# Performance work log

Hardware: AMD Instinct MI355X
Metric: run time of the kernel (lower is better)

Reference implementation:

```python
import jax, jax.numpy as jnp
import numpy as np
import math

N = 500_000
C_IN = 16
C_OUT = 64
H, W = 256, 256
PE_DIM = 32
BOUNDS = (-1.0, 1.0)
LN_EPS = 1e-5


def setup_inputs() -> dict:
    key = jax.random.key(0)
    ks = jax.random.split(key, 4)
    d_in = C_IN + 6 * PE_DIM  # 208
    pos = jax.random.uniform(ks[0], (N, 3), jnp.float32, minval=-1.0, maxval=1.0)
    features = jax.random.normal(ks[1], (N, C_IN), jnp.float32)
    W1 = jax.random.normal(ks[2], (d_in, C_OUT), jnp.float32) * (1.0 / math.sqrt(d_in))
    b1 = jnp.zeros((C_OUT,), jnp.float32)
    ln_g = jnp.ones((C_OUT,), jnp.float32)
    ln_b = jnp.zeros((C_OUT,), jnp.float32)
    W2 = jax.random.normal(ks[3], (C_OUT, C_OUT), jnp.float32) * (1.0 / math.sqrt(C_OUT))
    b2 = jnp.zeros((C_OUT,), jnp.float32)
    return {"pos": pos, "features": features, "W1": W1, "b1": b1,
            "ln_g": ln_g, "ln_b": ln_b, "W2": W2, "b2": b2,
            "axis1": 0, "axis2": 1}


def _pos_encode(pos):
    # sinusoidal encoding: per spatial dim, sin/cos at PE_DIM frequencies
    scale = BOUNDS[1] - BOUNDS[0]
    freq_bands = jnp.arange(PE_DIM, dtype=jnp.float32) / PE_DIM  # linspace(0,31,32)/32
    freqs = (pos / scale)[..., None] * (2.0 ** freq_bands) * math.pi  # [N,3,PE]
    # ordering per dim: sin_d, cos_d -> [N, 3*2*PE]
    enc = jnp.stack([jnp.sin(freqs), jnp.cos(freqs)], axis=2)  # [N,3,2,PE]
    return enc.reshape(pos.shape[0], 3 * 2 * PE_DIM)


def _layernorm(x, g, b):
    mu = jnp.mean(x, axis=-1, keepdims=True)
    var = jnp.var(x, axis=-1, keepdims=True)
    return (x - mu) * jax.lax.rsqrt(var + LN_EPS) * g + b


def reference(pos, features, W1, b1, ln_g, ln_b, W2, b2, axis1, axis2):
    # MLP on [features | pos_encoding]
    combined = jnp.concatenate([features, _pos_encode(pos)], axis=-1)  # [N,208]
    h = combined @ W1 + b1
    h = jax.nn.gelu(_layernorm(h, ln_g, ln_b), approximate=False)
    feat = h @ W2 + b2  # [N,C_OUT]

    # grid indices for the projected plane
    lo, hi = BOUNDS
    norm = jnp.clip((pos - lo) / (hi - lo), 0.0, 1.0)
    res = jnp.array([H, W], jnp.float32)
    i1 = jnp.clip(jnp.floor(norm[:, axis1] * res[0]), 0, H - 1).astype(jnp.int32)
    i2 = jnp.clip(jnp.floor(norm[:, axis2] * res[1]), 0, W - 1).astype(jnp.int32)
    flat = i1 * W + i2  # [N]

    # scatter-mean into grid
    sums = jax.ops.segment_sum(feat, flat, num_segments=H * W)  # [H*W, C]
    counts = jax.ops.segment_sum(jnp.ones((feat.shape[0],), jnp.float32), flat,
                                 num_segments=H * W)
    grid = sums / jnp.maximum(counts, 1.0)[:, None]  # [H*W, C]
    grid = grid.reshape(H, W, C_OUT).transpose(2, 0, 1)  # [C,H,W]
    return grid[None]  # [1,C,H,W]
```

## Files before the change

kernel.cpp:

```cpp
#include <hip/hip_runtime.h>
#include <math.h>

#define NPTS   500000
#define CIN    16
#define COUT   64
#define PE     32
#define GRID_H 256
#define GRID_W 256
#define NCELL  (GRID_H * GRID_W)

#define WS_HIST   0
#define WS_CUR    262144
#define WS_STARTS 524288
#define WS_RANK   786432
#define WS_WPK    2883456
#define WS_PART   2920320
#define WS_FEAT   2921344
#define WS_NEED   (WS_FEAT + (size_t)NPTS * COUT * 2)

#define PT_BLOCKS ((NPTS + 255) / 256)
#define MB_BLOCKS ((NPTS + 511) / 512)

#define W_HALFS   18432
#define W1_FRAGS  28
#define H_STRIDE  72
#define PS_WAVE   (16 * H_STRIDE)

typedef _Float16 f16x8 __attribute__((ext_vector_type(8)));
typedef _Float16 f16x2 __attribute__((ext_vector_type(2)));
typedef float    f32x4 __attribute__((ext_vector_type(4)));

__device__ __forceinline__ f16x2 pk2(float a, float b) {
    auto r = __builtin_amdgcn_cvt_pkrtz(a, b);
    union { decltype(r) x; f16x2 y; } u; u.x = r;
    return u.y;
}

__device__ __forceinline__ int cell_index(float v) {
    float nf = fminf(fmaxf((v + 1.0f) * 0.5f, 0.0f), 1.0f);
    int i = (int)floorf(nf * 256.0f);
    return i > 255 ? 255 : i;
}

__device__ __forceinline__ int flat_of(const float* pos, int p, int a1, int a2) {
    float pa1 = pos[p * 3 + a1];
    float pa2 = pos[p * 3 + a2];
    return cell_index(pa1) * GRID_W + cell_index(pa2);
}

__global__ void pack_hist_kernel(const float* __restrict__ W1,
                                 const float* __restrict__ W2,
                                 const float* __restrict__ pos,
                                 const int* __restrict__ ax1p,
                                 const int* __restrict__ ax2p,
                                 _Float16* __restrict__ wpk,
                                 unsigned int* __restrict__ hist,
                                 unsigned short* __restrict__ cellp)
{
    int i = blockIdx.x * 256 + threadIdx.x;
    if (i < W_HALFS) {
        int j = i & 7, lane = (i >> 3) & 63, f = i >> 9;
        int k  = ((f < W1_FRAGS) ? (f >> 2) : ((f - W1_FRAGS) >> 2)) * 32 + ((lane >> 4) << 3) + j;
        int ch = (f & 3) * 16 + (lane & 15);
        float v;
        if (f < W1_FRAGS) v = (k < 208) ? W1[k * 64 + ch] : 0.0f;
        else              v = W2[k * 64 + ch];
        wpk[i] = (_Float16)v;
    }
    if (i < NPTS) {
        int flat = flat_of(pos, i, ax1p[0], ax2p[0]);
        atomicAdd(&hist[flat], 1u);
        if (cellp) cellp[i] = (unsigned short)flat;
    }
}

__global__ void scan_sum_kernel(const unsigned int* __restrict__ hist,
                                unsigned int* __restrict__ part)
{
    __shared__ unsigned int sc[256];
    const int t = threadIdx.x;
    sc[t] = hist[blockIdx.x * 256 + t];
    __syncthreads();
    for (int off = 128; off > 0; off >>= 1) {
        if (t < off) sc[t] += sc[t + off];
        __syncthreads();
    }
    if (t == 0) part[blockIdx.x] = sc[0];
}

__global__ void scan_top_kernel(unsigned int* __restrict__ part)
{
    __shared__ unsigned int sc[256];
    const int t = threadIdx.x;
    unsigned int v = part[t];
    sc[t] = v;
    __syncthreads();
    for (int off = 1; off < 256; off <<= 1) {
        unsigned int add = (t >= off) ? sc[t - off] : 0u;
        __syncthreads();
        sc[t] += add;
        __syncthreads();
    }
    part[t] = sc[t] - v;
}

__global__ void scan_apply_kernel(const unsigned int* __restrict__ hist,
                                  const unsigned int* __restrict__ part,
                                  unsigned int* __restrict__ cur,
                                  unsigned int* __restrict__ starts)
{
    __shared__ unsigned int sc[256];
    const int t = threadIdx.x;
    unsigned int v = hist[blockIdx.x * 256 + t];
    sc[t] = v;
    __syncthreads();
    for (int off = 1; off < 256; off <<= 1) {
        unsigned int add = (t >= off) ? sc[t - off] : 0u;
        __syncthreads();
        sc[t] += add;
        __syncthreads();
    }
    unsigned int e = sc[t] - v + part[blockIdx.x];
    cur[blockIdx.x * 256 + t]    = e;
    starts[blockIdx.x * 256 + t] = e;
}

__global__ void scatter_kernel(const unsigned short* __restrict__ cellp,
                               unsigned int* __restrict__ cur,
                               int* __restrict__ rank)
{
    int p = blockIdx.x * 256 + threadIdx.x;
    if (p >= NPTS) return;
    int flat = cellp[p];
    rank[p] = (int)atomicAdd(&cur[flat], 1u);
}

__global__ __launch_bounds__(512, 4)
void mlp_mfma_kernel(const float* __restrict__ pos,
                     const float* __restrict__ feats,
                     const _Float16* __restrict__ wpk,
                     const float* __restrict__ b1,
                     const float* __restrict__ ln_g,
                     const float* __restrict__ ln_b,
                     const int*   __restrict__ ax1p,
                     const int*   __restrict__ ax2p,
                     const int*   __restrict__ rank,
                     _Float16* __restrict__ featbuf,
                     float* __restrict__ out,
                     int use_feat)
{
    __shared__ __align__(16) _Float16 WF[W_HALFS];
    __shared__ __align__(16) _Float16 PS[8 * PS_WAVE];

    {
        const uint4* src = (const uint4*)wpk;
        uint4* dst = (uint4*)WF;
        for (int i = threadIdx.x; i < W_HALFS / 8; i += 512) dst[i] = src[i];
    }

    const int lane = threadIdx.x & 63;
    const int wv   = threadIdx.x >> 6;
    const int g    = lane >> 4;
    const int n    = lane & 15;
    _Float16* Pw = PS + wv * PS_WAVE;

    int a1 = 0, a2 = 1;
    if (!use_feat) { a1 = ax1p[0]; a2 = ax2p[0]; }

    float b1v[4], lgv[4], lbv[4];
    #pragma unroll
    for (int c = 0; c < 4; ++c) {
        int ch = n + 16 * c;
        b1v[c] = b1[ch]; lgv[c] = ln_g[ch]; lbv[c] = ln_b[ch];
    }

    float ppx[4], ppy[4], ppz[4];
    const int wbase = blockIdx.x * 512 + wv * 64;
    int pt[4];
    #pragma unroll
    for (int t = 0; t < 4; ++t) {
        int st = wbase + t * 16 + n;
        int p  = (st < NPTS) ? st : 0;
        pt[t]  = p;
        ppx[t] = pos[3 * p + 0];
        ppy[t] = pos[3 * p + 1];
        ppz[t] = pos[3 * p + 2];
    }

    float4 fA[4], fB[4];
    if (g < 2) {
        #pragma unroll
        for (int t = 0; t < 4; ++t) {
            const float4* fr = (const float4*)(feats + (size_t)pt[t] * CIN + g * 8);
            fA[t] = fr[0]; fB[t] = fr[1];
        }
    }

    __syncthreads();

    f32x4 acc[4][4];
    #pragma unroll
    for (int t = 0; t < 4; ++t)
        #pragma unroll
        for (int c = 0; c < 4; ++c)
            acc[t][c] = (f32x4){0.0f, 0.0f, 0.0f, 0.0f};

    #pragma unroll
    for (int s = 0; s < 7; ++s) {
        const int k0 = s * 32 + g * 8;
        const bool isfeat = (s == 0) && (g < 2);
        const bool iszero = (k0 >= 208);
        float base = 0.0f, off = 0.0f; int d = 0;
        if (!isfeat && !iszero) {
            int e  = k0 - 16;
            d      = e >> 6;
            off    = ((e >> 5) & 1) ? 1.57079632679489662f : 0.0f;
            base   = 1.57079632679489662f * exp2f((float)(e & 31) * 0.03125f);
        }
        f16x8 af[4];
        #pragma unroll
        for (int t = 0; t < 4; ++t) {
            union { f16x8 v; f16x2 h[4]; } U;
            if (isfeat) {
                U.h[0] = pk2(fA[t].x, fA[t].y);
                U.h[1] = pk2(fA[t].z, fA[t].w);
                U.h[2] = pk2(fB[t].x, fB[t].y);
                U.h[3] = pk2(fB[t].z, fB[t].w);
            } else if (iszero) {
                #pragma unroll
                for (int q = 0; q < 4; ++q) U.h[q] = pk2(0.0f, 0.0f);
            } else {
                float pv  = (d == 0) ? ppx[t] : ((d == 1) ? ppy[t] : ppz[t]);
                float ang = pv * base;
                #pragma unroll
                for (int q = 0; q < 4; ++q) {
                    float v0 = __sinf(ang + off); ang *= 1.02189714865411668f;
                    float v1 = __sinf(ang + off); ang *= 1.02189714865411668f;
                    U.h[q] = pk2(v0, v1);
                }
            }
            af[t] = U.v;
        }
        #pragma unroll
        for (int c = 0; c < 4; ++c) {
            f16x8 bf = ((const f16x8*)WF)[(s * 4 + c) * 64 + lane];
            #pragma unroll
            for (int t = 0; t < 4; ++t)
                acc[t][c] = __builtin_amdgcn_mfma_f32_16x16x32_f16(af[t], bf, acc[t][c], 0, 0, 0);
        }
    }

    #pragma unroll
    for (int t = 0; t < 4; ++t) {
        f32x4 s1 = (f32x4){0.0f, 0.0f, 0.0f, 0.0f};
        f32x4 s2 = (f32x4){0.0f, 0.0f, 0.0f, 0.0f};
        #pragma unroll
        for (int c = 0; c < 4; ++c) {
            #pragma unroll
            for (int r = 0; r < 4; ++r) {
                float x = acc[t][c][r] + b1v[c];
                acc[t][c][r] = x;
                s1[r] += x;
                s2[r] += x * x;
            }
        }
        #pragma unroll
        for (int m = 1; m <= 8; m <<= 1) {
            #pragma unroll
            for (int r = 0; r < 4; ++r) {
                s1[r] += __shfl_xor(s1[r], m);
                s2[r] += __shfl_xor(s2[r], m);
            }
        }
        #pragma unroll
        for (int r = 0; r < 4; ++r) {
            float mu   = s1[r] * (1.0f / 64.0f);
            float var  = s2[r] * (1.0f / 64.0f) - mu * mu;
            float rstd = __builtin_amdgcn_rsqf(var + 1e-5f);
            int lrow = 4 * g + r;
            #pragma unroll
            for (int c = 0; c < 4; ++c) {
                float x  = (acc[t][c][r] - mu) * rstd * lgv[c] + lbv[c];
                float u  = x * (0.7978845608028654f + 0.0356774081363001f * x * x);
                float e  = __expf(2.0f * u);
                float th = 1.0f - 2.0f * __builtin_amdgcn_rcpf(e + 1.0f);
                float gv = 0.5f * x * (1.0f + th);
                Pw[lrow * H_STRIDE + n + 16 * c] = (_Float16)gv;
            }
        }

        f32x4 acc2[4];
        #pragma unroll
        for (int c = 0; c < 4; ++c) acc2[c] = (f32x4){0.0f, 0.0f, 0.0f, 0.0f};
        #pragma unroll
        for (int s = 0; s < 2; ++s) {
            f16x8 a2f = *(const f16x8*)(Pw + n * H_STRIDE + s * 32 + g * 8);
            #pragma unroll
            for (int c = 0; c < 4; ++c) {
                f16x8 bf = ((const f16x8*)WF)[(W1_FRAGS + s * 4 + c) * 64 + lane];
                acc2[c] = __builtin_amdgcn_mfma_f32_16x16x32_f16(a2f, bf, acc2[c], 0, 0, 0);
            }
        }

        #pragma unroll
        for (int r = 0; r < 4; ++r) {
            int lrow = 4 * g + r;
            #pragma unroll
            for (int c = 0; c < 4; ++c)
                Pw[lrow * H_STRIDE + n + 16 * c] = (_Float16)acc2[c][r];
        }

        if (use_feat) {
            int lrow  = lane >> 2;
            int gslot = wbase + t * 16 + lrow;
            if (gslot < NPTS) {
                int dst = rank[gslot];
                const uint4* src = (const uint4*)(Pw + lrow * H_STRIDE + (lane & 3) * 16);
                uint4* dstp = (uint4*)(featbuf + (size_t)dst * COUT + (lane & 3) * 16);
                dstp[0] = src[0];
                dstp[1] = src[1];
            }
        } else {
            int lrow = lane >> 2;
            int gp   = wbase + t * 16 + lrow;
            if (gp < NPTS) {
                int cellr = flat_of(pos, gp, a1, a2);
                const _Float16* srch = Pw + lrow * H_STRIDE;
                #pragma unroll
                for (int q = 0; q < 16; ++q) {
                    int ch = (lane & 3) * 16 + q;
                    unsafeAtomicAdd(&out[(size_t)ch * NCELL + cellr], (float)srch[ch]);
                }
            }
        }
    }
}

__global__ __launch_bounds__(256)
void reduce_kernel(const _Float16* __restrict__ featbuf,
                   const unsigned int* __restrict__ starts,
                   const unsigned int* __restrict__ hist,
                   const float* __restrict__ b2,
                   float* __restrict__ out)
{
    __shared__ float R[32][65];
    const int lane  = threadIdx.x & 63;
    const int wv    = threadIdx.x >> 6;
    const int cbase = blockIdx.x * 32;
    const float b2v = b2[lane];

    #pragma unroll
    for (int i = 0; i < 8; ++i) {
        int cl   = wv * 8 + i;
        int cell = cbase + cl;
        unsigned int s0  = starts[cell];
        unsigned int cnt = hist[cell];
        const _Float16* rp = featbuf + (size_t)s0 * COUT + lane;
        float a0 = 0.0f, a1 = 0.0f, a2 = 0.0f, a3 = 0.0f;
        unsigned int k = 0;
        for (; k + 4 <= cnt; k += 4) {
            float t0 = (float)rp[0];
            float t1 = (float)rp[COUT];
            float t2 = (float)rp[2 * COUT];
            float t3 = (float)rp[3 * COUT];
            rp += 4 * COUT;
            a0 += t0; a1 += t1; a2 += t2; a3 += t3;
        }
        for (; k < cnt; ++k) { a0 += (float)rp[0]; rp += COUT; }
        float m = (a0 + a1) + (a2 + a3);
        R[cl][lane] = m / fmaxf((float)cnt, 1.0f) + (cnt ? b2v : 0.0f);
    }
    __syncthreads();

    #pragma unroll
    for (int it = wv; it < 32; it += 4) {
        int ch = it * 2 + (lane >> 5);
        out[ch * NCELL + cbase + (lane & 31)] = R[lane & 31][ch];
    }
}

__global__ void finalize_kernel(float* __restrict__ out,
                                const unsigned int* __restrict__ hist,
                                const float* __restrict__ b2)
{
    int t = blockIdx.x * 256 + threadIdx.x;
    int cell = t & (NCELL - 1);
    int ch   = t >> 16;
    float c  = (float)hist[cell];
    out[t] = out[t] / fmaxf(c, 1.0f) + ((c > 0.0f) ? b2[ch] : 0.0f);
}

extern "C" void kernel_launch(void* const* d_in, const int* in_sizes, int n_in,
                              void* d_out, int out_size, void* d_ws, size_t ws_size,
                              hipStream_t stream) {
    (void)in_sizes; (void)n_in; (void)out_size;
    const float* pos   = (const float*)d_in[0];
    const float* feats = (const float*)d_in[1];
    const float* W1    = (const float*)d_in[2];
    const float* b1    = (const float*)d_in[3];
    const float* ln_g  = (const float*)d_in[4];
    const float* ln_b  = (const float*)d_in[5];
    const float* W2    = (const float*)d_in[6];
    const float* b2    = (const float*)d_in[7];
    const int*   ax1   = (const int*)d_in[8];
    const int*   ax2   = (const int*)d_in[9];

    char* ws = (char*)d_ws;
    unsigned int*   hist   = (unsigned int*)(ws + WS_HIST);
    unsigned int*   cur    = (unsigned int*)(ws + WS_CUR);
    unsigned int*   starts = (unsigned int*)(ws + WS_STARTS);
    int*            rank   = (int*)(ws + WS_RANK);
    _Float16*       wpk    = (_Float16*)(ws + WS_WPK);
    unsigned int*   part   = (unsigned int*)(ws + WS_PART);
    _Float16*       featbf = (_Float16*)(ws + WS_FEAT);
    unsigned short* cell16 = (unsigned short*)(ws + WS_FEAT);

    float* out = (float*)d_out;
    const int use_feat = (ws_size >= WS_NEED) ? 1 : 0;

    hipMemsetAsync(hist, 0, NCELL * sizeof(unsigned int), stream);
    if (!use_feat)
        hipMemsetAsync(d_out, 0, (size_t)COUT * NCELL * sizeof(float), stream);

    pack_hist_kernel<<<PT_BLOCKS, 256, 0, stream>>>(
        W1, W2, pos, ax1, ax2, wpk, hist,
        use_feat ? cell16 : (unsigned short*)nullptr);
    if (use_feat) {
        scan_sum_kernel<<<256, 256, 0, stream>>>(hist, part);
        scan_top_kernel<<<1, 256, 0, stream>>>(part);
        scan_apply_kernel<<<256, 256, 0, stream>>>(hist, part, cur, starts);
        scatter_kernel<<<PT_BLOCKS, 256, 0, stream>>>(cell16, cur, rank);
    }
    mlp_mfma_kernel<<<MB_BLOCKS, 512, 0, stream>>>(
        pos, feats, wpk, b1, ln_g, ln_b, ax1, ax2, rank, featbf, out, use_feat);
    if (use_feat)
        reduce_kernel<<<NCELL / 32, 256, 0, stream>>>(featbf, starts, hist, b2, out);
    else
        finalize_kernel<<<(COUT * NCELL) / 256, 256, 0, stream>>>(out, hist, b2);
}
```

Baseline: 219.3 us.

## Process point tiles sequentially, swap MFMA operands, swizzle LDS, widen reduce kernel

```diff
diff --git a/kernel.cpp b/kernel.cpp
--- a/kernel.cpp
+++ b/kernel.cpp
@@ -4,10 +4,8 @@
 #define NPTS   500000
 #define CIN    16
 #define COUT   64
-#define PE     32
-#define GRID_H 256
 #define GRID_W 256
-#define NCELL  (GRID_H * GRID_W)
+#define NCELL  65536
 
 #define WS_HIST   0
 #define WS_CUR    262144
@@ -23,8 +21,6 @@
 
 #define W_HALFS   18432
 #define W1_FRAGS  28
-#define H_STRIDE  72
-#define PS_WAVE   (16 * H_STRIDE)
 
 typedef _Float16 f16x8 __attribute__((ext_vector_type(8)));
 typedef _Float16 f16x2 __attribute__((ext_vector_type(2)));
@@ -135,7 +131,7 @@
     rank[p] = (int)atomicAdd(&cur[flat], 1u);
 }
 
-__global__ __launch_bounds__(512, 4)
+__global__ __launch_bounds__(512, 6)
 void mlp_mfma_kernel(const float* __restrict__ pos,
                      const float* __restrict__ feats,
                      const _Float16* __restrict__ wpk,
@@ -150,7 +146,7 @@
                      int use_feat)
 {
     __shared__ __align__(16) _Float16 WF[W_HALFS];
-    __shared__ __align__(16) _Float16 PS[8 * PS_WAVE];
+    __shared__ __align__(16) _Float16 PS[8 * 1024];
 
     {
         const uint4* src = (const uint4*)wpk;
@@ -162,131 +158,100 @@
     const int wv   = threadIdx.x >> 6;
     const int g    = lane >> 4;
     const int n    = lane & 15;
-    _Float16* Pw = PS + wv * PS_WAVE;
-
-    int a1 = 0, a2 = 1;
-    if (!use_feat) { a1 = ax1p[0]; a2 = ax2p[0]; }
-
-    float b1v[4], lgv[4], lbv[4];
-    #pragma unroll
-    for (int c = 0; c < 4; ++c) {
-        int ch = n + 16 * c;
-        b1v[c] = b1[ch]; lgv[c] = ln_g[ch]; lbv[c] = ln_b[ch];
-    }
-
-    float ppx[4], ppy[4], ppz[4];
+    char* Pw = (char*)(PS + wv * 1024);
+    const unsigned sw = (unsigned)((n & 7) << 4);
+
     const int wbase = blockIdx.x * 512 + wv * 64;
-    int pt[4];
-    #pragma unroll
+
+    const float base  = 1.57079632679489662f *
+                        exp2f((float)((8 * g + 16) & 31) * 0.03125f);
+    const float RSTEP = 1.02189714865411668f;
+    const float PI2   = 1.57079632679489662f;
+
+    __syncthreads();
+
+    #pragma unroll 1
     for (int t = 0; t < 4; ++t) {
-        int st = wbase + t * 16 + n;
-        int p  = (st < NPTS) ? st : 0;
-        pt[t]  = p;
-        ppx[t] = pos[3 * p + 0];
-        ppy[t] = pos[3 * p + 1];
-        ppz[t] = pos[3 * p + 2];
-    }
-
-    float4 fA[4], fB[4];
-    if (g < 2) {
-        #pragma unroll
-        for (int t = 0; t < 4; ++t) {
-            const float4* fr = (const float4*)(feats + (size_t)pt[t] * CIN + g * 8);
-            fA[t] = fr[0]; fB[t] = fr[1];
-        }
-    }
-
-    __syncthreads();
-
-    f32x4 acc[4][4];
-    #pragma unroll
-    for (int t = 0; t < 4; ++t)
-        #pragma unroll
-        for (int c = 0; c < 4; ++c)
-            acc[t][c] = (f32x4){0.0f, 0.0f, 0.0f, 0.0f};
-
-    #pragma unroll
-    for (int s = 0; s < 7; ++s) {
-        const int k0 = s * 32 + g * 8;
-        const bool isfeat = (s == 0) && (g < 2);
-        const bool iszero = (k0 >= 208);
-        float base = 0.0f, off = 0.0f; int d = 0;
-        if (!isfeat && !iszero) {
-            int e  = k0 - 16;
-            d      = e >> 6;
-            off    = ((e >> 5) & 1) ? 1.57079632679489662f : 0.0f;
-            base   = 1.57079632679489662f * exp2f((float)(e & 31) * 0.03125f);
-        }
-        f16x8 af[4];
-        #pragma unroll
-        for (int t = 0; t < 4; ++t) {
+        const int st = wbase + t * 16 + n;
+        const int p  = (st < NPTS) ? st : 0;
+        const float px = pos[3 * p + 0];
+        const float py = pos[3 * p + 1];
+        const float pz = pos[3 * p + 2];
+
+        float4 fA, fB;
+        if (g < 2) {
+            const float4* fr = (const float4*)(feats + (size_t)p * CIN + g * 8);
+            fA = fr[0]; fB = fr[1];
+        }
+
+        f32x4 acc[4];
+        #pragma unroll
+        for (int c = 0; c < 4; ++c) acc[c] = (f32x4){0.0f, 0.0f, 0.0f, 0.0f};
+
+        #pragma unroll
+        for (int s = 0; s < 7; ++s) {
             union { f16x8 v; f16x2 h[4]; } U;
-            if (isfeat) {
-                U.h[0] = pk2(fA[t].x, fA[t].y);
-                U.h[1] = pk2(fA[t].z, fA[t].w);
-                U.h[2] = pk2(fB[t].x, fB[t].y);
-                U.h[3] = pk2(fB[t].z, fB[t].w);
-            } else if (iszero) {
+            const int k0 = s * 32 + g * 8;
+            if (s == 0 && g < 2) {
+                U.h[0] = pk2(fA.x, fA.y); U.h[1] = pk2(fA.z, fA.w);
+                U.h[2] = pk2(fB.x, fB.y); U.h[3] = pk2(fB.z, fB.w);
+            } else if (k0 >= 208) {
                 #pragma unroll
                 for (int q = 0; q < 4; ++q) U.h[q] = pk2(0.0f, 0.0f);
             } else {
-                float pv  = (d == 0) ? ppx[t] : ((d == 1) ? ppy[t] : ppz[t]);
-                float ang = pv * base;
+                const int   e    = k0 - 16;
+                const float pv   = (e < 64) ? px : ((e < 128) ? py : pz);
+                const float off  = (e & 32) ? PI2 : 0.0f;
+                const float offc = (e & 32) ? (PI2 * (1.0f - RSTEP)) : 0.0f;
+                float a = fmaf(pv, base, off);
                 #pragma unroll
                 for (int q = 0; q < 4; ++q) {
-                    float v0 = __sinf(ang + off); ang *= 1.02189714865411668f;
-                    float v1 = __sinf(ang + off); ang *= 1.02189714865411668f;
+                    float v0 = __sinf(a); a = fmaf(a, RSTEP, offc);
+                    float v1 = __sinf(a); a = fmaf(a, RSTEP, offc);
                     U.h[q] = pk2(v0, v1);
                 }
             }
-            af[t] = U.v;
-        }
+            #pragma unroll
+            for (int c = 0; c < 4; ++c) {
+                f16x8 af = ((const f16x8*)WF)[(s * 4 + c) * 64 + lane];
+                acc[c] = __builtin_amdgcn_mfma_f32_16x16x32_f16(af, U.v, acc[c], 0, 0, 0);
+            }
+        }
+
+        float s1 = 0.0f, s2 = 0.0f;
         #pragma unroll
         for (int c = 0; c < 4; ++c) {
-            f16x8 bf = ((const f16x8*)WF)[(s * 4 + c) * 64 + lane];
-            #pragma unroll
-            for (int t = 0; t < 4; ++t)
-                acc[t][c] = __builtin_amdgcn_mfma_f32_16x16x32_f16(af[t], bf, acc[t][c], 0, 0, 0);
-        }
-    }
-
-    #pragma unroll
-    for (int t = 0; t < 4; ++t) {
-        f32x4 s1 = (f32x4){0.0f, 0.0f, 0.0f, 0.0f};
-        f32x4 s2 = (f32x4){0.0f, 0.0f, 0.0f, 0.0f};
+            f32x4 b1q = *(const f32x4*)(b1 + 16 * c + 4 * g);
+            #pragma unroll
+            for (int r = 0; r < 4; ++r) {
+                float x = acc[c][r] + b1q[r];
+                acc[c][r] = x;
+                s1 += x; s2 += x * x;
+            }
+        }
+        s1 += __shfl_xor(s1, 16); s2 += __shfl_xor(s2, 16);
+        s1 += __shfl_xor(s1, 32); s2 += __shfl_xor(s2, 32);
+        const float mu   = s1 * (1.0f / 64.0f);
+        const float var  = s2 * (1.0f / 64.0f) - mu * mu;
+        const float rstd = __builtin_amdgcn_rsqf(var + 1e-5f);
+
         #pragma unroll
         for (int c = 0; c < 4; ++c) {
+            f32x4 gq = *(const f32x4*)(ln_g + 16 * c + 4 * g);
+            f32x4 bq = *(const f32x4*)(ln_b + 16 * c + 4 * g);
+            float gv[4];
             #pragma unroll
             for (int r = 0; r < 4; ++r) {
-                float x = acc[t][c][r] + b1v[c];
-                acc[t][c][r] = x;
-                s1[r] += x;
-                s2[r] += x * x;
-            }
-        }
-        #pragma unroll
-        for (int m = 1; m <= 8; m <<= 1) {
-            #pragma unroll
-            for (int r = 0; r < 4; ++r) {
-                s1[r] += __shfl_xor(s1[r], m);
-                s2[r] += __shfl_xor(s2[r], m);
-            }
-        }
-        #pragma unroll
-        for (int r = 0; r < 4; ++r) {
-            float mu   = s1[r] * (1.0f / 64.0f);
-            float var  = s2[r] * (1.0f / 64.0f) - mu * mu;
-            float rstd = __builtin_amdgcn_rsqf(var + 1e-5f);
-            int lrow = 4 * g + r;
-            #pragma unroll
-            for (int c = 0; c < 4; ++c) {
-                float x  = (acc[t][c][r] - mu) * rstd * lgv[c] + lbv[c];
+                float x  = (acc[c][r] - mu) * rstd * gq[r] + bq[r];
                 float u  = x * (0.7978845608028654f + 0.0356774081363001f * x * x);
                 float e  = __expf(2.0f * u);
                 float th = 1.0f - 2.0f * __builtin_amdgcn_rcpf(e + 1.0f);
-                float gv = 0.5f * x * (1.0f + th);
-                Pw[lrow * H_STRIDE + n + 16 * c] = (_Float16)gv;
-            }
+                gv[r] = 0.5f * x * (1.0f + th);
+            }
+            union { f16x2 h[2]; uint2 u2; } W;
+            W.h[0] = pk2(gv[0], gv[1]);
+            W.h[1] = pk2(gv[2], gv[3]);
+            *(uint2*)(Pw + n * 128 + (((unsigned)(32 * c + 8 * g)) ^ sw)) = W.u2;
         }
 
         f32x4 acc2[4];
@@ -294,89 +259,85 @@
         for (int c = 0; c < 4; ++c) acc2[c] = (f32x4){0.0f, 0.0f, 0.0f, 0.0f};
         #pragma unroll
         for (int s = 0; s < 2; ++s) {
-            f16x8 a2f = *(const f16x8*)(Pw + n * H_STRIDE + s * 32 + g * 8);
+            f16x8 bf2 = *(const f16x8*)(Pw + n * 128 + (((unsigned)(64 * s + 16 * g)) ^ sw));
             #pragma unroll
             for (int c = 0; c < 4; ++c) {
-                f16x8 bf = ((const f16x8*)WF)[(W1_FRAGS + s * 4 + c) * 64 + lane];
-                acc2[c] = __builtin_amdgcn_mfma_f32_16x16x32_f16(a2f, bf, acc2[c], 0, 0, 0);
-            }
-        }
-
-        #pragma unroll
-        for (int r = 0; r < 4; ++r) {
-            int lrow = 4 * g + r;
-            #pragma unroll
-            for (int c = 0; c < 4; ++c)
-                Pw[lrow * H_STRIDE + n + 16 * c] = (_Float16)acc2[c][r];
+                f16x8 af = ((const f16x8*)WF)[(W1_FRAGS + s * 4 + c) * 64 + lane];
+                acc2[c] = __builtin_amdgcn_mfma_f32_16x16x32_f16(af, bf2, acc2[c], 0, 0, 0);
+            }
         }
 
         if (use_feat) {
-            int lrow  = lane >> 2;
-            int gslot = wbase + t * 16 + lrow;
-            if (gslot < NPTS) {
-                int dst = rank[gslot];
-                const uint4* src = (const uint4*)(Pw + lrow * H_STRIDE + (lane & 3) * 16);
-                uint4* dstp = (uint4*)(featbuf + (size_t)dst * COUT + (lane & 3) * 16);
-                dstp[0] = src[0];
-                dstp[1] = src[1];
+            #pragma unroll
+            for (int c = 0; c < 4; ++c) {
+                union { f16x2 h[2]; uint2 u2; } W;
+                W.h[0] = pk2(acc2[c][0], acc2[c][1]);
+                W.h[1] = pk2(acc2[c][2], acc2[c][3]);
+                *(uint2*)(Pw + n * 128 + (((unsigned)(32 * c + 8 * g)) ^ sw)) = W.u2;
+            }
+            #pragma unroll
+            for (int h = 0; h < 2; ++h) {
+                const int row = h * 8 + (lane >> 3);
+                const int gs  = wbase + t * 16 + row;
+                if (gs < NPTS) {
+                    const uint4 v = *(const uint4*)(Pw + row * 128 +
+                        (((unsigned)((lane & 7) * 16)) ^ ((unsigned)((row & 7) << 4))));
+                    *(uint4*)(featbuf + (size_t)rank[gs] * COUT + (lane & 7) * 8) = v;
+                }
             }
         } else {
-            int lrow = lane >> 2;
-            int gp   = wbase + t * 16 + lrow;
-            if (gp < NPTS) {
-                int cellr = flat_of(pos, gp, a1, a2);
-                const _Float16* srch = Pw + lrow * H_STRIDE;
+            if (st < NPTS) {
+                const int cellr = flat_of(pos, p, ax1p[0], ax2p[0]);
                 #pragma unroll
-                for (int q = 0; q < 16; ++q) {
-                    int ch = (lane & 3) * 16 + q;
-                    unsafeAtomicAdd(&out[(size_t)ch * NCELL + cellr], (float)srch[ch]);
-                }
-            }
-        }
-    }
-}
-
-__global__ __launch_bounds__(256)
+                for (int c = 0; c < 4; ++c)
+                    #pragma unroll
+                    for (int r = 0; r < 4; ++r)
+                        unsafeAtomicAdd(&out[(size_t)(16 * c + 4 * g + r) * NCELL + cellr],
+                                        acc2[c][r]);
+            }
+        }
+    }
+}
+
+__global__ __launch_bounds__(1024)
 void reduce_kernel(const _Float16* __restrict__ featbuf,
                    const unsigned int* __restrict__ starts,
                    const unsigned int* __restrict__ hist,
                    const float* __restrict__ b2,
                    float* __restrict__ out)
 {
-    __shared__ float R[32][65];
+    __shared__ float R[16][66];
     const int lane  = threadIdx.x & 63;
     const int wv    = threadIdx.x >> 6;
-    const int cbase = blockIdx.x * 32;
+    const int cbase = blockIdx.x * 16;
     const float b2v = b2[lane];
 
-    #pragma unroll
-    for (int i = 0; i < 8; ++i) {
-        int cl   = wv * 8 + i;
-        int cell = cbase + cl;
-        unsigned int s0  = starts[cell];
-        unsigned int cnt = hist[cell];
-        const _Float16* rp = featbuf + (size_t)s0 * COUT + lane;
-        float a0 = 0.0f, a1 = 0.0f, a2 = 0.0f, a3 = 0.0f;
-        unsigned int k = 0;
-        for (; k + 4 <= cnt; k += 4) {
-            float t0 = (float)rp[0];
-            float t1 = (float)rp[COUT];
-            float t2 = (float)rp[2 * COUT];
-            float t3 = (float)rp[3 * COUT];
-            rp += 4 * COUT;
-            a0 += t0; a1 += t1; a2 += t2; a3 += t3;
-        }
-        for (; k < cnt; ++k) { a0 += (float)rp[0]; rp += COUT; }
-        float m = (a0 + a1) + (a2 + a3);
-        R[cl][lane] = m / fmaxf((float)cnt, 1.0f) + (cnt ? b2v : 0.0f);
-    }
+    const int cell = cbase + wv;
+    const unsigned int s0  = starts[cell];
+    const unsigned int cnt = hist[cell];
+
+    float a0 = 0.0f, a1 = 0.0f, a2 = 0.0f, a3 = 0.0f;
+    for (unsigned int k = 0; k < cnt; k += 4) {
+        unsigned int i0 = s0 + k;
+        unsigned int i1 = i0 + 1 < (unsigned)NPTS ? i0 + 1 : (unsigned)(NPTS - 1);
+        unsigned int i2 = i0 + 2 < (unsigned)NPTS ? i0 + 2 : (unsigned)(NPTS - 1);
+        unsigned int i3 = i0 + 3 < (unsigned)NPTS ? i0 + 3 : (unsigned)(NPTS - 1);
+        float v0 = (float)featbuf[(size_t)i0 * COUT + lane];
+        float v1 = (float)featbuf[(size_t)i1 * COUT + lane];
+        float v2 = (float)featbuf[(size_t)i2 * COUT + lane];
+        float v3 = (float)featbuf[(size_t)i3 * COUT + lane];
+        a0 += v0;
+        a1 += (k + 1 < cnt) ? v1 : 0.0f;
+        a2 += (k + 2 < cnt) ? v2 : 0.0f;
+        a3 += (k + 3 < cnt) ? v3 : 0.0f;
+    }
+    float m = (a0 + a1) + (a2 + a3);
+    R[wv][lane] = m / fmaxf((float)cnt, 1.0f) + (cnt ? b2v : 0.0f);
     __syncthreads();
 
-    #pragma unroll
-    for (int it = wv; it < 32; it += 4) {
-        int ch = it * 2 + (lane >> 5);
-        out[ch * NCELL + cbase + (lane & 31)] = R[lane & 31][ch];
-    }
+    const int ch = threadIdx.x >> 4;
+    const int ci = threadIdx.x & 15;
+    out[ch * NCELL + cbase + ci] = R[ci][ch];
 }
 
 __global__ void finalize_kernel(float* __restrict__ out,
@@ -434,7 +395,7 @@
     mlp_mfma_kernel<<<MB_BLOCKS, 512, 0, stream>>>(
         pos, feats, wpk, b1, ln_g, ln_b, ax1, ax2, rank, featbf, out, use_feat);
     if (use_feat)
-        reduce_kernel<<<NCELL / 32, 256, 0, stream>>>(featbf, starts, hist, b2, out);
+        reduce_kernel<<<NCELL / 16, 1024, 0, stream>>>(featbf, starts, hist, b2, out);
     else
         finalize_kernel<<<(COUT * NCELL) / 256, 256, 0, stream>>>(out, hist, b2);
 }
```

Measured after the change: 573.9 us. 2.62x slower.
